# Kernel optimization log

Hardware: AMD Instinct MI355X
Metric: run time of the kernel (lower is better)

Reference implementation:

```python
import jax, jax.numpy as jnp
import numpy as np

ZERO = 1e-8
L = 2            # num_gnn_layers
D = 256          # dim_node_features
B = 32           # graphs per batch
NPG = 256        # nodes per graph
N = B * NPG      # total nodes
E = 131072       # edges per edge-type
MAX_TOKENS = 256 # MAX_TOKENS_OF_A_POST
UPD = 0.5        # args.updated_weights_for_A


def _make_edges(k):
    k1, k2, k3 = jax.random.split(k, 3)
    g = jax.random.randint(k1, (E,), 0, B) * NPG          # keep edges within a graph
    src = g + jax.random.randint(k2, (E,), 0, NPG)
    dst = g + jax.random.randint(k3, (E,), 0, NPG)
    return jnp.stack([src, dst]).astype(jnp.int64)


def setup_inputs() -> dict:
    key = jax.random.key(0)
    ks = jax.random.split(key, 12)
    x = jax.random.normal(ks[0], (N, D), dtype=jnp.float32)
    ei_e = _make_edges(ks[1]); ew_e = jax.random.uniform(ks[2], (E,), dtype=jnp.float32)
    ei_p = _make_edges(ks[3]); ew_p = jax.random.uniform(ks[4], (E,), dtype=jnp.float32)
    ei_o = _make_edges(ks[5]); ew_o = jax.random.uniform(ks[6], (E,), dtype=jnp.float32)
    entity_mask = jax.random.randint(ks[7], (B, NPG), 0, 2).astype(bool)
    pattern_mask = jax.random.randint(ks[8], (B, NPG), 0, 2).astype(bool)
    s = 1.0 / np.sqrt(D)
    W_gcn = (jax.random.normal(ks[9], (L, 3, D, D), dtype=jnp.float32) * s)
    b_gcn = jnp.zeros((L, 3, D), dtype=jnp.float32)
    T_dyn = (jax.random.normal(ks[10], (L, D, D), dtype=jnp.float32) * s)
    return {
        'x': x,
        'edge_index_entity': ei_e, 'edge_weight_entity': ew_e,
        'edge_index_pattern': ei_p, 'edge_weight_pattern': ew_p,
        'edge_index_others': ei_o, 'edge_weight_others': ew_o,
        'entity_mask': entity_mask, 'pattern_mask': pattern_mask,
        'W_gcn': W_gcn, 'b_gcn': b_gcn, 'T_dyn': T_dyn,
    }


def _normalized_correlation_matrix(H):
    # cosine-similarity correlation matrix, symmetrically degree-normalized
    nrm = jnp.sqrt(jnp.sum(H * H, axis=1))
    A = (H @ H.T) / (nrm[:, None] * nrm[None, :] + ZERO)
    dinv = 1.0 / jnp.sqrt(jnp.abs(jnp.sum(A, axis=1)) + ZERO)
    return dinv[:, None] * A * dinv[None, :]


def _gcn(H, W, b, ei, ew):
    # GCNConv(add_self_loops=False, normalize=False): scatter-sum of weighted source messages
    msg = (H @ W)[ei[0]] * ew[:, None]                     # [E, D]
    return jax.ops.segment_sum(msg, ei[1], num_segments=N) + b


def _forward(x, we0, wp0, wo0, W_gcn, b_gcn, T_dyn,
             ei_e, ei_p, ei_o, entity_mask, pattern_mask):
    H = x
    A = _normalized_correlation_matrix(H)                  # [N, N]
    for i in range(L):
        if i == 0:
            we, wp, wo = we0, wp0, wo0
        else:
            # diag(one_hot(src) @ A @ one_hot(dst).T) == A[src, dst]
            we = A[ei_e[0], ei_e[1]]
            wp = A[ei_p[0], ei_p[1]]
            wo = A[ei_o[0], ei_o[1]]
        He = _gcn(H, W_gcn[i, 0], b_gcn[i, 0], ei_e, we)
        Hp = _gcn(H, W_gcn[i, 1], b_gcn[i, 1], ei_p, wp)
        Ho = _gcn(H, W_gcn[i, 2], b_gcn[i, 2], ei_o, wo)
        H = jax.nn.relu(He + Hp + Ho)
        A_hat = jax.nn.sigmoid((H @ T_dyn[i]) @ H.T)
        A = (1.0 - UPD) * A + UPD * A_hat
    # per-graph diagonal blocks of A  -> [B, NPG, NPG]
    A4 = A.reshape(B, NPG, B, NPG)
    idx = jnp.arange(B)
    blocks = A4[idx, :, idx, :]
    A_sum = jnp.sum(blocks, axis=-1)                       # [B, NPG]
    ent_cols = jnp.einsum('bij,bj->bi', blocks, entity_mask.astype(A.dtype))
    pat_cols = jnp.einsum('bij,bj->bi', blocks, pattern_mask.astype(A.dtype))
    map_pattern = A_sum - ent_cols
    map_entity = A_sum - pat_cols

    def finish(m):
        mn = jnp.min(m, axis=1, keepdims=True)
        mx = jnp.max(m, axis=1, keepdims=True)
        m = (m - mn) / (mx - mn + ZERO)
        m = m / (jnp.sum(m, axis=1, keepdims=True) + ZERO)
        return m[:, :MAX_TOKENS]                           # padding() with NPG==MAX_TOKENS

    return finish(map_entity), finish(map_pattern)


def reference(x, edge_index_entity, edge_weight_entity,
              edge_index_pattern, edge_weight_pattern,
              edge_index_others, edge_weight_others,
              entity_mask, pattern_mask, W_gcn, b_gcn, T_dyn):
    return _forward(x, edge_weight_entity, edge_weight_pattern, edge_weight_others,
                    W_gcn, b_gcn, T_dyn,
                    edge_index_entity, edge_index_pattern, edge_index_others,
                    entity_mask, pattern_mask)
```

## Files before the change

kernel.cpp:

```cpp
#include <hip/hip_runtime.h>

#define NND   8192
#define DDIM  256
#define NGRP  32
#define ZEROF 1e-8f
#define LSTR  40
#define TSTR  72
#define OFF_AH 0
#define OFF_AL 2560
#define OFF_BH 5120
#define OFF_BL 10240
#define OFF_TT 5120
#define LDS_U16 16384

typedef unsigned short u16;
typedef __attribute__((ext_vector_type(8))) short short8v;
typedef __attribute__((ext_vector_type(4))) float float4v;

__device__ inline u16 f2bf(float x) {
  unsigned u = __float_as_uint(x);
  u += 0x7fffu + ((u >> 16) & 1u);
  return (u16)(u >> 16);
}
__device__ inline float bf2f(u16 h) { return __uint_as_float((unsigned)h << 16); }
__device__ inline void split2(float x, u16& h, u16& l) {
  h = f2bf(x);
  l = f2bf(x - bf2f(h));
}

__device__ inline float wave_sum(float v) {
#pragma unroll
  for (int off = 32; off > 0; off >>= 1) v += __shfl_down(v, off, 64);
  return v;
}

#define LOAD_REGS(tt, kk)                                                                   \
  {                                                                                         \
    int m_ = tid >> 2, kq_ = (tid & 3) * 8;                                                 \
    size_t aoff_;                                                                           \
    if (MODE == 1)                                                                          \
      aoff_ = (size_t)((tt) * 256 + bym * 64 + m_) * 8192 + (size_t)(g * 256 + (kk) + kq_); \
    else if (MODE == 2 || MODE == 3)                                                        \
      aoff_ = (size_t)(g * 256 + bym * 64 + m_) * 256 + (kk) + kq_;                         \
    else                                                                                    \
      aoff_ = (size_t)(bym * 64 + m_) * 256 + (kk) + kq_;                                   \
    rAh = *(const short8v*)&Ah_g[aoff_];                                                    \
    rAl = *(const short8v*)&Al_g[aoff_];                                                    \
    size_t bbase_ = (MODE == 1) ? ((size_t)(g * 3 + (tt)) << 16)                            \
                  : ((MODE == 2 || MODE == 3) ? ((size_t)g << 16) : (size_t)0);             \
    if (HALF) {                                                                             \
      int n_ = tid & 63, kq2_ = (tid >> 6) * 8;                                             \
      size_t boff_ = bbase_ + (size_t)(col0 + n_) * 256 + (kk) + kq2_;                      \
      rBh0 = *(const short8v*)&Bh_g[boff_];                                                 \
      rBl0 = *(const short8v*)&Bl_g[boff_];                                                 \
    } else {                                                                                \
      int n_ = tid & 127, kq2_ = (tid >> 7) * 16;                                           \
      size_t boff_ = bbase_ + (size_t)(col0 + n_) * 256 + (kk) + kq2_;                      \
      rBh0 = *(const short8v*)&Bh_g[boff_]; rBh1 = *(const short8v*)&Bh_g[boff_ + 8];       \
      rBl0 = *(const short8v*)&Bl_g[boff_]; rBl1 = *(const short8v*)&Bl_g[boff_ + 8];       \
    }                                                                                       \
  }

template<int MODE, bool HALF>
__device__ __forceinline__ void mfma_body(
    u16* lds,
    const u16* __restrict__ Ah_g, const u16* __restrict__ Al_g,
    const u16* __restrict__ Bh_g, const u16* __restrict__ Bl_g,
    float* __restrict__ Cf, u16* __restrict__ Ch, u16* __restrict__ Cl,
    const float* __restrict__ nrm, const float* __restrict__ dinv,
    const float* __restrict__ bias,
    int bxm, int bym, int g) {
  u16* Ahs = lds + OFF_AH;
  u16* Als = lds + OFF_AL;
  u16* Bhs = lds + OFF_BH;
  u16* Bls = lds + OFF_BL;
  u16* Tt  = lds + OFF_TT;
  const int NJ = HALF ? 2 : 4;
  const int tid = threadIdx.x;
  const int col0 = bxm * (HALF ? 64 : 128);
  const int w = tid >> 6, lane = tid & 63;
  const int lm = lane & 15, lq = lane >> 4;
  const int wr = (w >> 1) * 32, wc = (w & 1) * (HALF ? 32 : 64);

  float4v acc[2][4];
#pragma unroll
  for (int i = 0; i < 2; ++i)
#pragma unroll
    for (int j = 0; j < NJ; ++j) acc[i][j] = (float4v)0.f;

  short8v rAh, rAl, rBh0, rBh1, rBl0, rBl1;
  const int TOTAL = (MODE == 1) ? 24 : 8;

  LOAD_REGS(0, 0);
  for (int step = 0; step < TOTAL; ++step) {
    if (step) __syncthreads();
    {
      int m = tid >> 2, kq = (tid & 3) * 8;
      *(short8v*)&Ahs[m * LSTR + kq] = rAh;
      *(short8v*)&Als[m * LSTR + kq] = rAl;
    }
    if (HALF) {
      int n = tid & 63, kq2 = (tid >> 6) * 8;
      *(short8v*)&Bhs[n * LSTR + kq2] = rBh0;
      *(short8v*)&Bls[n * LSTR + kq2] = rBl0;
    } else {
      int n = tid & 127, kq2 = (tid >> 7) * 16;
      *(short8v*)&Bhs[n * LSTR + kq2] = rBh0; *(short8v*)&Bhs[n * LSTR + kq2 + 8] = rBh1;
      *(short8v*)&Bls[n * LSTR + kq2] = rBl0; *(short8v*)&Bls[n * LSTR + kq2 + 8] = rBl1;
    }
    int nxt = step + 1;
    if (nxt < TOTAL) {
      int tt = nxt >> 3, kk = (nxt & 7) * 32;
      LOAD_REGS(tt, kk);
    }
    __syncthreads();
    short8v ah[2], al[2], bh[4], bl[4];
#pragma unroll
    for (int i = 0; i < 2; ++i) {
      int r = wr + i * 16 + lm;
      ah[i] = *(const short8v*)&Ahs[r * LSTR + lq * 8];
      al[i] = *(const short8v*)&Als[r * LSTR + lq * 8];
    }
#pragma unroll
    for (int j = 0; j < NJ; ++j) {
      int r = wc + j * 16 + lm;
      bh[j] = *(const short8v*)&Bhs[r * LSTR + lq * 8];
      bl[j] = *(const short8v*)&Bls[r * LSTR + lq * 8];
    }
#pragma unroll
    for (int i = 0; i < 2; ++i)
#pragma unroll
      for (int j = 0; j < NJ; ++j) {
        acc[i][j] = __builtin_amdgcn_mfma_f32_16x16x32_bf16(ah[i], bh[j], acc[i][j], 0, 0, 0);
        acc[i][j] = __builtin_amdgcn_mfma_f32_16x16x32_bf16(ah[i], bl[j], acc[i][j], 0, 0, 0);
        acc[i][j] = __builtin_amdgcn_mfma_f32_16x16x32_bf16(al[i], bh[j], acc[i][j], 0, 0, 0);
      }
  }

  if (MODE == 2 || MODE == 3) {
#pragma unroll
    for (int i = 0; i < 2; ++i) {
#pragma unroll
      for (int r = 0; r < 4; ++r) {
        int grow = g * 256 + bym * 64 + wr + i * 16 + lq * 4 + r;
        float di = 0.f, ni = 0.f;
        if (MODE == 2) { di = dinv[grow]; ni = nrm[grow]; }
#pragma unroll
        for (int j = 0; j < NJ; ++j) {
          int gcol = col0 + wc + j * 16 + lm;
          size_t ci = (size_t)grow * 256 + gcol;
          float v = acc[i][j][r];
          if (MODE == 2) {
            int gj = g * 256 + gcol;
            Cf[ci] = v * di * dinv[gj] / (ni * nrm[gj] + ZEROF);
          } else {
            Cf[ci] = 0.5f * Cf[ci] + 0.5f * (1.f / (1.f + expf(-v)));
          }
        }
      }
    }
  } else {
    float bsum[8];
    if (MODE == 1) {
#pragma unroll
      for (int i = 0; i < 2; ++i)
#pragma unroll
        for (int r = 0; r < 4; ++r) {
          int d = bym * 64 + wr + i * 16 + lq * 4 + r;
          bsum[i * 4 + r] = bias[d] + bias[256 + d] + bias[512 + d];
        }
    }
    u16 hv[32], lv[32];
#pragma unroll
    for (int i = 0; i < 2; ++i)
#pragma unroll
      for (int j = 0; j < NJ; ++j)
#pragma unroll
        for (int r = 0; r < 4; ++r) {
          float v = acc[i][j][r];
          if (MODE == 1) v = fmaxf(v + bsum[i * 4 + r], 0.f);
          split2(v, hv[(i * 4 + r) * NJ + j], lv[(i * 4 + r) * NJ + j]);
        }
    int ebase1 = (MODE == 1) ? (g * 256 + col0) : col0;
    int ebase2 = bym * 64;
    size_t estride = (MODE == 0) ? 8192 : 256;
#pragma unroll
    for (int ph = 0; ph < 2; ++ph) {
      __syncthreads();
      const u16* sv = ph ? lv : hv;
#pragma unroll
      for (int i = 0; i < 2; ++i)
#pragma unroll
        for (int j = 0; j < NJ; ++j)
#pragma unroll
          for (int r = 0; r < 4; ++r)
            Tt[(wc + j * 16 + lm) * TSTR + wr + i * 16 + lq * 4 + r] = sv[(i * 4 + r) * NJ + j];
      __syncthreads();
      u16* dst = ph ? Cl : Ch;
      int cc0 = tid >> 3, mm0 = (tid & 7) * 8;
#pragma unroll
      for (int it = 0; it < (HALF ? 2 : 4); ++it) {
        int cc = it * 32 + cc0;
        short8v v = *(const short8v*)&Tt[cc * TSTR + mm0];
        *(short8v*)&dst[(size_t)(ebase1 + cc) * estride + ebase2 + mm0] = v;
      }
    }
  }
}

__device__ __forceinline__ void mbuild_body(
    float* tile, int bid, int l,
    const u16* __restrict__ sct, const uint2* __restrict__ recs, int nBkt,
    const float* __restrict__ Abuf, u16* __restrict__ Mbh, u16* __restrict__ Mbl) {
  const int tid = threadIdx.x;
  int gt = bid >> 3, chunk = bid & 7;
  int g = gt / 3;
  float4 z = make_float4(0.f, 0.f, 0.f, 0.f);
#pragma unroll
  for (int k = 0; k < 8; ++k) ((float4*)tile)[k * 256 + tid] = z;
  __syncthreads();
  for (int bb = tid; bb < nBkt; bb += 256) {
    unsigned sc = sct[(size_t)bb * 768 + bid];
    unsigned start = sc & 2047u, cnt = sc >> 11;
    const uint2* rp = &recs[(size_t)bb * 768 + start];
    for (unsigned k = 0; k < cnt; ++k) {
      uint2 r = rp[k];
      int s = r.x & 255, d5 = (r.x >> 8) & 31;
      float w = l ? Abuf[(size_t)(g * 256 + s) * 256 + chunk * 32 + d5]
                  : __uint_as_float(r.y);
      atomicAdd(&tile[d5 * 256 + s], w);
    }
  }
  __syncthreads();
  size_t base4 = ((size_t)gt << 14) + ((size_t)chunk << 11);
#pragma unroll
  for (int k = 0; k < 8; ++k) {
    float4 f = ((float4*)tile)[k * 256 + tid];
    ushort4 h, lo;
    split2(f.x, h.x, lo.x); split2(f.y, h.y, lo.y);
    split2(f.z, h.z, lo.z); split2(f.w, h.w, lo.w);
    ((ushort4*)Mbh)[base4 + k * 256 + tid] = h;
    ((ushort4*)Mbl)[base4 + k * 256 + tid] = lo;
  }
}

__global__ void k_prep(const int* __restrict__ e0, const int* __restrict__ e1,
                       const int* __restrict__ e2, const unsigned char* __restrict__ m0,
                       const unsigned char* __restrict__ m1,
                       const float* __restrict__ W, const float* __restrict__ T,
                       const float* __restrict__ x,
                       const float* __restrict__ ew0, const float* __restrict__ ew1,
                       const float* __restrict__ ew2,
                       float* __restrict__ emf, float* __restrict__ pmf,
                       u16* __restrict__ Wth, u16* __restrict__ Wtl,
                       u16* __restrict__ sct, uint2* __restrict__ recs,
                       float* __restrict__ nrm, float* __restrict__ Spart,
                       u16* __restrict__ Hh, u16* __restrict__ Hl,
                       int E_, int nCvt, int nBkt) {
  __shared__ float tile[32][33];
  __shared__ float inv[64];
  __shared__ int nz[1];
  __shared__ unsigned int hcnt[768];
  __shared__ unsigned int hoff[768];
  __shared__ unsigned int ppart[256];
  __shared__ uint2 stage[768];
  const int b = blockIdx.x, tid = threadIdx.x;
  if (b < nCvt) {
    if (tid == 0) nz[0] = 0;
    __syncthreads();
    int i4 = tid * 4;
    int c = (m0[i4 + 1] != 0) + (m0[i4 + 2] != 0) + (m0[i4 + 3] != 0);
    if (c) atomicAdd(&nz[0], c);
    __syncthreads();
    int fM = (nz[0] == 0);
    int i = b * 256 + tid;
    if (i < NND) {
      unsigned char v = fM ? m0[4 * i] : m0[i];
      emf[i] = 1.f - (float)(v != 0);
    } else {
      int j = i - NND;
      unsigned char v = fM ? m1[4 * j] : m1[j];
      pmf[j] = 1.f - (float)(v != 0);
    }
  } else if (b < nCvt + nBkt) {
    if (tid == 0) nz[0] = 0;
    hcnt[tid] = 0; hcnt[tid + 256] = 0; hcnt[tid + 512] = 0;
    __syncthreads();
    if (e0[2 * tid + 1] != 0) atomicAdd(&nz[0], 1);
    __syncthreads();
    int fE = (nz[0] == 0);
    int e = (b - nCvt) * 256 + tid;
    bool valid = (e < E_);
    int mybid[3]; unsigned int myrec[3]; float myw[3];
    if (valid) {
#pragma unroll
      for (int t = 0; t < 3; ++t) {
        const int* ei = (t == 0) ? e0 : ((t == 1) ? e1 : e2);
        int src = fE ? ei[2 * e] : ei[e];
        int dst = fE ? ei[2 * (E_ + e)] : ei[E_ + e];
        int g = src >> 8, s = src & 255, d = dst & 255;
        mybid[t] = ((g * 3 + t) << 3) | (d >> 5);
        myrec[t] = (unsigned)(((d & 31) << 8) | s);
        myw[t] = (t == 0 ? ew0 : (t == 1 ? ew1 : ew2))[e];
        atomicAdd(&hcnt[mybid[t]], 1u);
      }
    }
    __syncthreads();
    unsigned c0 = hcnt[3 * tid], c1 = hcnt[3 * tid + 1], c2 = hcnt[3 * tid + 2];
    unsigned tsum = c0 + c1 + c2;
    ppart[tid] = tsum;
    __syncthreads();
    for (int off = 1; off < 256; off <<= 1) {
      unsigned v = (tid >= off) ? ppart[tid - off] : 0u;
      __syncthreads();
      ppart[tid] += v;
      __syncthreads();
    }
    unsigned base = ppart[tid] - tsum;
    hoff[3 * tid] = base;
    hoff[3 * tid + 1] = base + c0;
    hoff[3 * tid + 2] = base + c0 + c1;
    __syncthreads();
#pragma unroll
    for (int k = 0; k < 3; ++k) {
      int bin = tid + k * 256;
      unsigned cc = hcnt[bin]; if (cc > 31u) cc = 31u;
      sct[(size_t)(b - nCvt) * 768 + bin] = (u16)(hoff[bin] | (cc << 11));
    }
    __syncthreads();
    if (valid) {
#pragma unroll
      for (int t = 0; t < 3; ++t) {
        unsigned slot = atomicAdd(&hoff[mybid[t]], 1u);
        stage[slot] = make_uint2(myrec[t], __float_as_uint(myw[t]));
      }
    }
    __syncthreads();
    uint2* dstp = &recs[(size_t)(b - nCvt) * 768];
    dstp[tid] = stage[tid];
    dstp[tid + 256] = stage[tid + 256];
    dstp[tid + 512] = stage[tid + 512];
  } else if (b < nCvt + nBkt + 512) {
    int bb = b - nCvt - nBkt;
    int mat = bb >> 6, rem = bb & 63;
    int k0 = (rem >> 3) * 32, n0 = (rem & 7) * 32;
    const float* src = (mat < 6) ? (W + (size_t)mat * 65536) : (T + (size_t)(mat - 6) * 65536);
    int r = tid >> 3, c4 = (tid & 7) * 4;
    const float4 v = *(const float4*)&src[(size_t)(k0 + r) * 256 + n0 + c4];
    tile[r][c4 + 0] = v.x; tile[r][c4 + 1] = v.y; tile[r][c4 + 2] = v.z; tile[r][c4 + 3] = v.w;
    __syncthreads();
    float o[4] = {tile[c4 + 0][r], tile[c4 + 1][r], tile[c4 + 2][r], tile[c4 + 3][r]};
    u16 hh[4], ll[4];
#pragma unroll
    for (int q = 0; q < 4; ++q) split2(o[q], hh[q], ll[q]);
    size_t off = (size_t)mat * 65536 + (size_t)(n0 + r) * 256 + k0 + c4;
    *(ushort4*)&Wth[off] = *(ushort4*)hh;
    *(ushort4*)&Wtl[off] = *(ushort4*)ll;
  } else {
    int bn = b - nCvt - nBkt - 512;
    int n0 = bn * 64;
    int w = tid >> 6, lane = tid & 63;
    for (int it = 0; it < 16; ++it) {
      int nl = it * 4 + w;
      int node = n0 + nl;
      const float4 v = *(const float4*)&x[(size_t)node * 256 + lane * 4];
      u16 hh[4], ll[4];
      split2(v.x, hh[0], ll[0]); split2(v.y, hh[1], ll[1]);
      split2(v.z, hh[2], ll[2]); split2(v.w, hh[3], ll[3]);
      *(ushort4*)&Hh[(size_t)node * 256 + lane * 4] = *(ushort4*)hh;
      *(ushort4*)&Hl[(size_t)node * 256 + lane * 4] = *(ushort4*)ll;
      float s = wave_sum(v.x * v.x + v.y * v.y + v.z * v.z + v.w * v.w);
      if (lane == 0) { float nr = sqrtf(s); nrm[node] = nr; inv[nl] = 1.f / nr; }
    }
    __syncthreads();
    float s = 0.f;
    for (int i = 0; i < 64; ++i) s += x[(size_t)(n0 + i) * 256 + tid] * inv[i];
    Spart[bn * 256 + tid] = s;
  }
}

__global__ __launch_bounds__(256, 2) void k_stageA(
    const u16* __restrict__ Hinh, const u16* __restrict__ Hinl,
    const u16* __restrict__ Wth, const u16* __restrict__ Wtl,
    u16* __restrict__ XWTh, u16* __restrict__ XWTl,
    const u16* __restrict__ sct, const uint2* __restrict__ recs, int nBkt,
    u16* __restrict__ Mbh, u16* __restrict__ Mbl,
    const float* __restrict__ x, const float* __restrict__ Spart,
    const float* __restrict__ nrm, float* __restrict__ dinv) {
  __shared__ u16 lds[LDS_U16];
  const int b = blockIdx.x;
  if (b < 768) {
    mfma_body<0, false>(lds, Hinh, Hinl, Wth, Wtl,
                        nullptr, XWTh, XWTl, nullptr, nullptr, nullptr,
                        b >> 7, b & 127, 0);
  } else if (b < 1536) {
    mbuild_body((float*)lds, b - 768, 0, sct, recs, nBkt, nullptr, Mbh, Mbl);
  } else {
    float* Sl = (float*)lds;
    const int tid = threadIdx.x;
    float s = 0.f;
    for (int bb = 0; bb < 128; ++bb) s += Spart[bb * 256 + tid];
    Sl[tid] = s;
    __syncthreads();
    int base = (b - 1536) * 64;
    int w = tid >> 6, lane = tid & 63;
    const float4 sv = *(const float4*)&Sl[lane * 4];
    for (int it = 0; it < 16; ++it) {
      int node = base + it * 4 + w;
      const float4 v = *(const float4*)&x[(size_t)node * 256 + lane * 4];
      float s2 = wave_sum(v.x * sv.x + v.y * sv.y + v.z * sv.z + v.w * sv.w);
      if (lane == 0) {
        float rowsum = s2 / nrm[node];
        dinv[node] = rsqrtf(fabsf(rowsum) + ZEROF);
      }
    }
  }
}

__global__ __launch_bounds__(256, 2) void k_stageA2(
    const u16* __restrict__ H2h, const u16* __restrict__ H2l,
    const u16* __restrict__ Wth, const u16* __restrict__ Wtl,
    u16* __restrict__ XWTh, u16* __restrict__ XWTl,
    const u16* __restrict__ sct, const uint2* __restrict__ recs, int nBkt,
    const float* __restrict__ Abuf,
    u16* __restrict__ Mbh, u16* __restrict__ Mbl) {
  __shared__ u16 lds[LDS_U16];
  const int b = blockIdx.x;
  if (b < 768) {
    mfma_body<0, false>(lds, H2h, H2l, Wth + (size_t)768 * 256, Wtl + (size_t)768 * 256,
                        nullptr, XWTh, XWTl, nullptr, nullptr, nullptr,
                        b >> 7, b & 127, 0);
  } else {
    mbuild_body((float*)lds, b - 768, 1, sct, recs, nBkt, Abuf, Mbh, Mbl);
  }
}

__global__ __launch_bounds__(256, 2) void k_stageB(
    const u16* __restrict__ XWTh, const u16* __restrict__ XWTl,
    const u16* __restrict__ Mbh, const u16* __restrict__ Mbl,
    u16* __restrict__ Houth, u16* __restrict__ Houtl, const float* __restrict__ bias,
    const u16* __restrict__ xh, const u16* __restrict__ xl, float* __restrict__ Abuf,
    const float* __restrict__ nrm, const float* __restrict__ dinv) {
  __shared__ u16 lds[LDS_U16];
  const int b = blockIdx.x;
  if (b < 512) {
    int g = b & 31, r = b >> 5;
    mfma_body<1, true>(lds, XWTh, XWTl, Mbh, Mbl,
                       nullptr, Houth, Houtl, nullptr, nullptr, bias,
                       r >> 2, r & 3, g);
  } else {
    int bb = b - 512;
    int g = bb & 31, r = bb >> 5;
    mfma_body<2, true>(lds, xh, xl, xh, xl, Abuf, nullptr, nullptr,
                       nrm, dinv, nullptr, r >> 2, r & 3, g);
  }
}

__global__ __launch_bounds__(256, 2) void k_stageC(
    const u16* __restrict__ Wth, const u16* __restrict__ Wtl, int l,
    const u16* __restrict__ Hh, const u16* __restrict__ Hl,
    u16* __restrict__ tmph, u16* __restrict__ tmpl) {
  __shared__ u16 lds[LDS_U16];
  const int b = blockIdx.x;
  mfma_body<4, true>(lds, Wth + (size_t)(6 + l) * 65536, Wtl + (size_t)(6 + l) * 65536,
                     Hh, Hl, nullptr, tmph, tmpl, nullptr, nullptr, nullptr,
                     b & 127, b >> 7, 0);
}

__global__ __launch_bounds__(256, 2) void k_stageD(
    const u16* __restrict__ tmph, const u16* __restrict__ tmpl,
    const u16* __restrict__ Hh, const u16* __restrict__ Hl,
    float* __restrict__ Abuf) {
  __shared__ u16 lds[LDS_U16];
  const int b = blockIdx.x;
  int g = b & 31, r = b >> 5;
  mfma_body<3, true>(lds, tmph, tmpl, Hh, Hl, Abuf, nullptr, nullptr,
                     nullptr, nullptr, nullptr, r >> 2, r & 3, g);
}

__global__ void k_maps(const float* __restrict__ Abuf, const float* __restrict__ emf,
                       const float* __restrict__ pmf, float* __restrict__ out) {
  __shared__ float sme[256], smp[256], red[256];
  const int g = blockIdx.x, tid = threadIdx.x, w = tid >> 6, lane = tid & 63;
  const int j0 = g * 256 + lane * 4;
  const float4 pmv = *(const float4*)&pmf[j0];
  const float4 emv = *(const float4*)&emf[j0];
  for (int it = 0; it < 64; ++it) {
    int nl = it * 4 + w;
    const float4 a = *(const float4*)&Abuf[((size_t)g * 256 + nl) * 256 + lane * 4];
    float me = a.x * pmv.x + a.y * pmv.y + a.z * pmv.z + a.w * pmv.w;
    float mp = a.x * emv.x + a.y * emv.y + a.z * emv.z + a.w * emv.w;
#pragma unroll
    for (int off = 32; off > 0; off >>= 1) {
      me += __shfl_down(me, off, 64);
      mp += __shfl_down(mp, off, 64);
    }
    if (lane == 0) { sme[nl] = me; smp[nl] = mp; }
  }
  __syncthreads();
  for (int which = 0; which < 2; ++which) {
    float v = which ? smp[tid] : sme[tid];
    red[tid] = v; __syncthreads();
    for (int s = 128; s > 0; s >>= 1) { if (tid < s) red[tid] = fminf(red[tid], red[tid + s]); __syncthreads(); }
    float mn = red[0]; __syncthreads();
    red[tid] = v; __syncthreads();
    for (int s = 128; s > 0; s >>= 1) { if (tid < s) red[tid] = fmaxf(red[tid], red[tid + s]); __syncthreads(); }
    float mx = red[0]; __syncthreads();
    float m = (v - mn) / (mx - mn + ZEROF);
    red[tid] = m; __syncthreads();
    for (int s = 128; s > 0; s >>= 1) { if (tid < s) red[tid] += red[tid + s]; __syncthreads(); }
    float sum = red[0]; __syncthreads();
    out[which * NND + g * 256 + tid] = m / (sum + ZEROF);
  }
}

extern "C" void kernel_launch(void* const* d_in, const int* in_sizes, int n_in,
                              void* d_out, int out_size, void* d_ws, size_t ws_size,
                              hipStream_t stream) {
  const float* x = (const float*)d_in[0];
  const unsigned char* em_raw = (const unsigned char*)d_in[7];
  const unsigned char* pm_raw = (const unsigned char*)d_in[8];
  const float* W  = (const float*)d_in[9];
  const float* bg = (const float*)d_in[10];
  const float* T  = (const float*)d_in[11];
  float* out = (float*)d_out;
  const int E_ = in_sizes[2];

  const int nCvt = (2 * NND) / 256;
  const int nBkt = (E_ + 255) / 256;

  float* ws = (float*)d_ws;
  size_t o = 0;
  float* Abuf = ws + o; o += (size_t)NND * 256;
  u16* Mbh_l0 = (u16*)(ws + o); o += (size_t)NGRP * 3 * 65536 / 2;
  u16* Mbl_l0 = (u16*)(ws + o); o += (size_t)NGRP * 3 * 65536 / 2;
  u16* Mbh_l1 = (u16*)(ws + o); o += (size_t)NGRP * 3 * 65536 / 2;
  u16* Mbl_l1 = (u16*)(ws + o); o += (size_t)NGRP * 3 * 65536 / 2;
  u16* Hh   = (u16*)(ws + o); o += (size_t)NND * 256 / 2;
  u16* Hl   = (u16*)(ws + o); o += (size_t)NND * 256 / 2;
  u16* H2h  = (u16*)(ws + o); o += (size_t)NND * 256 / 2;
  u16* H2l  = (u16*)(ws + o); o += (size_t)NND * 256 / 2;
  u16* tmph = (u16*)(ws + o); o += (size_t)NND * 256 / 2;
  u16* tmpl = (u16*)(ws + o); o += (size_t)NND * 256 / 2;
  u16* XWTh = (u16*)(ws + o); o += (size_t)768 * NND / 2;
  u16* XWTl = (u16*)(ws + o); o += (size_t)768 * NND / 2;
  u16* Wth  = (u16*)(ws + o); o += (size_t)8 * 65536 / 2;
  u16* Wtl  = (u16*)(ws + o); o += (size_t)8 * 65536 / 2;
  float* nrm   = ws + o; o += NND;
  float* dinv  = ws + o; o += NND;
  float* Spart = ws + o; o += 128 * 256;
  float* emf   = ws + o; o += NND;
  float* pmf   = ws + o; o += NND;
  u16* sct     = (u16*)(ws + o); o += (size_t)nBkt * 768 / 2;
  uint2* recs  = (uint2*)(ws + o); o += (size_t)nBkt * 768 * 2;

  const float* ew0 = (const float*)d_in[2];
  const float* ew1 = (const float*)d_in[4];
  const float* ew2 = (const float*)d_in[6];

  k_prep<<<nCvt + nBkt + 512 + 128, 256, 0, stream>>>(
      (const int*)d_in[1], (const int*)d_in[3], (const int*)d_in[5], em_raw, pm_raw,
      W, T, x, ew0, ew1, ew2, emf, pmf, Wth, Wtl, sct, recs,
      nrm, Spart, Hh, Hl, E_, nCvt, nBkt);

  k_stageA<<<1664, 256, 0, stream>>>(Hh, Hl, Wth, Wtl, XWTh, XWTl,
                                     sct, recs, nBkt, Mbh_l0, Mbl_l0,
                                     x, Spart, nrm, dinv);
  k_stageB<<<1024, 256, 0, stream>>>(XWTh, XWTl, Mbh_l0, Mbl_l0, H2h, H2l, bg,
                                     Hh, Hl, Abuf, nrm, dinv);
  k_stageC<<<512, 256, 0, stream>>>(Wth, Wtl, 0, H2h, H2l, tmph, tmpl);
  k_stageD<<<512, 256, 0, stream>>>(tmph, tmpl, H2h, H2l, Abuf);

  k_stageA2<<<1536, 256, 0, stream>>>(H2h, H2l, Wth, Wtl, XWTh, XWTl,
                                      sct, recs, nBkt, Abuf, Mbh_l1, Mbl_l1);
  k_stageB<<<512, 256, 0, stream>>>(XWTh, XWTl, Mbh_l1, Mbl_l1, Hh, Hl, bg + 768,
                                    nullptr, nullptr, nullptr, nullptr, nullptr);
  k_stageC<<<512, 256, 0, stream>>>(Wth, Wtl, 1, Hh, Hl, tmph, tmpl);
  k_stageD<<<512, 256, 0, stream>>>(tmph, tmpl, Hh, Hl, Abuf);

  k_maps<<<NGRP, 256, 0, stream>>>(Abuf, emf, pmf, out);
}
```

Baseline: 276.9 us.

## Move raw H·Hᵀ block GEMM into stage A and defer normalization to stage D

The per-graph correlation GEMM (MODE 2) moves from stage B into the stage-A grid, so it runs alongside the XW GEMMs and M-build, and it now stores unnormalized values. The cosine/degree scaling is folded into the first stage-D epilogue (new MODE 5). Stage A computes dinv, which stage B previously read, so deferring the scaling lets the GEMM start earlier and shrinks stage B to only the GCN GEMM. The __syncthreads in the main loop also moves before the next-tile global prefetch, changing the load/compute overlap.

Result: no change. 274.6 us (-0.9%).

```diff
diff --git a/kernel.cpp b/kernel.cpp
--- a/kernel.cpp
+++ b/kernel.cpp
@@ -40,14 +40,14 @@
     size_t aoff_;                                                                           \
     if (MODE == 1)                                                                          \
       aoff_ = (size_t)((tt) * 256 + bym * 64 + m_) * 8192 + (size_t)(g * 256 + (kk) + kq_); \
-    else if (MODE == 2 || MODE == 3)                                                        \
+    else if (MODE == 2 || MODE == 3 || MODE == 5)                                           \
       aoff_ = (size_t)(g * 256 + bym * 64 + m_) * 256 + (kk) + kq_;                         \
     else                                                                                    \
       aoff_ = (size_t)(bym * 64 + m_) * 256 + (kk) + kq_;                                   \
     rAh = *(const short8v*)&Ah_g[aoff_];                                                    \
     rAl = *(const short8v*)&Al_g[aoff_];                                                    \
     size_t bbase_ = (MODE == 1) ? ((size_t)(g * 3 + (tt)) << 16)                            \
-                  : ((MODE == 2 || MODE == 3) ? ((size_t)g << 16) : (size_t)0);             \
+                  : ((MODE == 2 || MODE == 3 || MODE == 5) ? ((size_t)g << 16) : (size_t)0);\
     if (HALF) {                                                                             \
       int n_ = tid & 63, kq2_ = (tid >> 6) * 8;                                             \
       size_t boff_ = bbase_ + (size_t)(col0 + n_) * 256 + (kk) + kq2_;                      \
@@ -108,12 +108,12 @@
       *(short8v*)&Bhs[n * LSTR + kq2] = rBh0; *(short8v*)&Bhs[n * LSTR + kq2 + 8] = rBh1;
       *(short8v*)&Bls[n * LSTR + kq2] = rBl0; *(short8v*)&Bls[n * LSTR + kq2 + 8] = rBl1;
     }
+    __syncthreads();
     int nxt = step + 1;
     if (nxt < TOTAL) {
       int tt = nxt >> 3, kk = (nxt & 7) * 32;
       LOAD_REGS(tt, kk);
     }
-    __syncthreads();
     short8v ah[2], al[2], bh[4], bl[4];
 #pragma unroll
     for (int i = 0; i < 2; ++i) {
@@ -137,24 +137,27 @@
       }
   }
 
-  if (MODE == 2 || MODE == 3) {
+  if (MODE == 2 || MODE == 3 || MODE == 5) {
 #pragma unroll
     for (int i = 0; i < 2; ++i) {
 #pragma unroll
       for (int r = 0; r < 4; ++r) {
         int grow = g * 256 + bym * 64 + wr + i * 16 + lq * 4 + r;
         float di = 0.f, ni = 0.f;
-        if (MODE == 2) { di = dinv[grow]; ni = nrm[grow]; }
+        if (MODE == 5) { di = dinv[grow]; ni = nrm[grow]; }
 #pragma unroll
         for (int j = 0; j < NJ; ++j) {
           int gcol = col0 + wc + j * 16 + lm;
           size_t ci = (size_t)grow * 256 + gcol;
           float v = acc[i][j][r];
           if (MODE == 2) {
+            Cf[ci] = v;
+          } else if (MODE == 3) {
+            Cf[ci] = 0.5f * Cf[ci] + 0.5f * (1.f / (1.f + expf(-v)));
+          } else {
             int gj = g * 256 + gcol;
-            Cf[ci] = v * di * dinv[gj] / (ni * nrm[gj] + ZEROF);
-          } else {
-            Cf[ci] = 0.5f * Cf[ci] + 0.5f * (1.f / (1.f + expf(-v)));
+            float scale = di * dinv[gj] / (ni * nrm[gj] + ZEROF);
+            Cf[ci] = 0.5f * Cf[ci] * scale + 0.5f * (1.f / (1.f + expf(-v)));
           }
         }
       }
@@ -385,6 +388,7 @@
     u16* __restrict__ XWTh, u16* __restrict__ XWTl,
     const u16* __restrict__ sct, const uint2* __restrict__ recs, int nBkt,
     u16* __restrict__ Mbh, u16* __restrict__ Mbl,
+    float* __restrict__ Abuf,
     const float* __restrict__ x, const float* __restrict__ Spart,
     const float* __restrict__ nrm, float* __restrict__ dinv) {
   __shared__ u16 lds[LDS_U16];
@@ -395,6 +399,11 @@
                         b >> 7, b & 127, 0);
   } else if (b < 1536) {
     mbuild_body((float*)lds, b - 768, 0, sct, recs, nBkt, nullptr, Mbh, Mbl);
+  } else if (b < 2048) {
+    int bb = b - 1536;
+    int g = bb & 31, r = bb >> 5;
+    mfma_body<2, true>(lds, Hinh, Hinl, Hinh, Hinl, Abuf, nullptr, nullptr,
+                       nullptr, nullptr, nullptr, r >> 2, r & 3, g);
   } else {
     float* Sl = (float*)lds;
     const int tid = threadIdx.x;
@@ -402,7 +411,7 @@
     for (int bb = 0; bb < 128; ++bb) s += Spart[bb * 256 + tid];
     Sl[tid] = s;
     __syncthreads();
-    int base = (b - 1536) * 64;
+    int base = (b - 2048) * 64;
     int w = tid >> 6, lane = tid & 63;
     const float4 sv = *(const float4*)&Sl[lane * 4];
     for (int it = 0; it < 16; ++it) {
@@ -438,22 +447,13 @@
 __global__ __launch_bounds__(256, 2) void k_stageB(
     const u16* __restrict__ XWTh, const u16* __restrict__ XWTl,
     const u16* __restrict__ Mbh, const u16* __restrict__ Mbl,
-    u16* __restrict__ Houth, u16* __restrict__ Houtl, const float* __restrict__ bias,
-    const u16* __restrict__ xh, const u16* __restrict__ xl, float* __restrict__ Abuf,
-    const float* __restrict__ nrm, const float* __restrict__ dinv) {
+    u16* __restrict__ Houth, u16* __restrict__ Houtl, const float* __restrict__ bias) {
   __shared__ u16 lds[LDS_U16];
   const int b = blockIdx.x;
-  if (b < 512) {
-    int g = b & 31, r = b >> 5;
-    mfma_body<1, true>(lds, XWTh, XWTl, Mbh, Mbl,
-                       nullptr, Houth, Houtl, nullptr, nullptr, bias,
-                       r >> 2, r & 3, g);
-  } else {
-    int bb = b - 512;
-    int g = bb & 31, r = bb >> 5;
-    mfma_body<2, true>(lds, xh, xl, xh, xl, Abuf, nullptr, nullptr,
-                       nrm, dinv, nullptr, r >> 2, r & 3, g);
-  }
+  int g = b & 31, r = b >> 5;
+  mfma_body<1, true>(lds, XWTh, XWTl, Mbh, Mbl,
+                     nullptr, Houth, Houtl, nullptr, nullptr, bias,
+                     r >> 2, r & 3, g);
 }
 
 __global__ __launch_bounds__(256, 2) void k_stageC(
@@ -470,12 +470,17 @@
 __global__ __launch_bounds__(256, 2) void k_stageD(
     const u16* __restrict__ tmph, const u16* __restrict__ tmpl,
     const u16* __restrict__ Hh, const u16* __restrict__ Hl,
-    float* __restrict__ Abuf) {
+    float* __restrict__ Abuf,
+    const float* __restrict__ nrm, const float* __restrict__ dinv, int scaled) {
   __shared__ u16 lds[LDS_U16];
   const int b = blockIdx.x;
   int g = b & 31, r = b >> 5;
-  mfma_body<3, true>(lds, tmph, tmpl, Hh, Hl, Abuf, nullptr, nullptr,
-                     nullptr, nullptr, nullptr, r >> 2, r & 3, g);
+  if (scaled)
+    mfma_body<5, true>(lds, tmph, tmpl, Hh, Hl, Abuf, nullptr, nullptr,
+                       nrm, dinv, nullptr, r >> 2, r & 3, g);
+  else
+    mfma_body<3, true>(lds, tmph, tmpl, Hh, Hl, Abuf, nullptr, nullptr,
+                       nullptr, nullptr, nullptr, r >> 2, r & 3, g);
 }
 
 __global__ void k_maps(const float* __restrict__ Abuf, const float* __restrict__ emf,
@@ -563,20 +568,18 @@
       W, T, x, ew0, ew1, ew2, emf, pmf, Wth, Wtl, sct, recs,
       nrm, Spart, Hh, Hl, E_, nCvt, nBkt);
 
-  k_stageA<<<1664, 256, 0, stream>>>(Hh, Hl, Wth, Wtl, XWTh, XWTl,
-                                     sct, recs, nBkt, Mbh_l0, Mbl_l0,
+  k_stageA<<<2176, 256, 0, stream>>>(Hh, Hl, Wth, Wtl, XWTh, XWTl,
+                                     sct, recs, nBkt, Mbh_l0, Mbl_l0, Abuf,
                                      x, Spart, nrm, dinv);
-  k_stageB<<<1024, 256, 0, stream>>>(XWTh, XWTl, Mbh_l0, Mbl_l0, H2h, H2l, bg,
-                                     Hh, Hl, Abuf, nrm, dinv);
+  k_stageB<<<512, 256, 0, stream>>>(XWTh, XWTl, Mbh_l0, Mbl_l0, H2h, H2l, bg);
   k_stageC<<<512, 256, 0, stream>>>(Wth, Wtl, 0, H2h, H2l, tmph, tmpl);
-  k_stageD<<<512, 256, 0, stream>>>(tmph, tmpl, H2h, H2l, Abuf);
+  k_stageD<<<512, 256, 0, stream>>>(tmph, tmpl, H2h, H2l, Abuf, nrm, dinv, 1);
 
   k_stageA2<<<1536, 256, 0, stream>>>(H2h, H2l, Wth, Wtl, XWTh, XWTl,
                                       sct, recs, nBkt, Abuf, Mbh_l1, Mbl_l1);
-  k_stageB<<<512, 256, 0, stream>>>(XWTh, XWTl, Mbh_l1, Mbl_l1, Hh, Hl, bg + 768,
-                                    nullptr, nullptr, nullptr, nullptr, nullptr);
+  k_stageB<<<512, 256, 0, stream>>>(XWTh, XWTl, Mbh_l1, Mbl_l1, Hh, Hl, bg + 768);
   k_stageC<<<512, 256, 0, stream>>>(Wth, Wtl, 1, Hh, Hl, tmph, tmpl);
-  k_stageD<<<512, 256, 0, stream>>>(tmph, tmpl, Hh, Hl, Abuf);
+  k_stageD<<<512, 256, 0, stream>>>(tmph, tmpl, Hh, Hl, Abuf, nullptr, nullptr, 0);
 
   k_maps<<<NGRP, 256, 0, stream>>>(Abuf, emf, pmf, out);
 }
```
